# Performance work log

Hardware: AMD Instinct MI355X
Metric: run time of the kernel (lower is better)

The kernel has to match this reference:

```python
import jax, jax.numpy as jnp
import numpy as np

DIM = 768
NUM_HEADS = 12


def setup_inputs() -> dict:
    key = jax.random.key(0)
    k1, k2, k3 = jax.random.split(key, 3)
    x = jax.random.normal(k1, (8, 32, 32, DIM), dtype=jnp.float32)
    # xavier_uniform-style init for kernels
    lim_qkv = float(np.sqrt(6.0 / (DIM + 3 * DIM)))
    lim_o = float(np.sqrt(6.0 / (DIM + DIM)))
    w_qkv = jax.random.uniform(k2, (DIM, 3 * DIM), jnp.float32, -lim_qkv, lim_qkv)
    w_o = jax.random.uniform(k3, (DIM, DIM), jnp.float32, -lim_o, lim_o)
    return {"x": x, "w_qkv": w_qkv, "w_o": w_o}


def reference(x, w_qkv, w_o):
    bs, h, w, c = x.shape
    n = h * w
    nh = NUM_HEADS
    hd = c // nh
    xt = x.reshape(bs, n, c)
    qkv = xt @ w_qkv                                   # [bs, n, 3c]
    qkv = qkv.reshape(bs, n, 3, nh, hd)
    qkv = jnp.transpose(qkv, (2, 0, 3, 1, 4))          # [3, bs, nh, n, hd]
    q, k, v = qkv[0], qkv[1], qkv[2]
    scale = hd ** -0.5
    attn = jnp.einsum('bhqd,bhkd->bhqk', q, k) * scale  # [bs, nh, n, n]
    attn = jax.nn.softmax(attn, axis=-1)
    out = jnp.einsum('bhqk,bhkd->bhqd', attn, v)       # [bs, nh, n, hd]
    out = out.swapaxes(1, 2).reshape(bs, n, c)
    out = out @ w_o
    side = int(n ** 0.5)
    return out.reshape(bs, side, side, -1)
```

## Files before the change

kernel.cpp:

```cpp
#include <hip/hip_runtime.h>
#include <hip/hip_bf16.h>
#include <stdint.h>
#include <math.h>

#define SEQ   1024
#define NHEAD 12
#define HD    64
#define CDIM  768
#define MTOK  8192
#define NQKV  2304
#define NPAIR 96

#define QSCALE 0.18033688011112042f

typedef uint16_t u16;
typedef __attribute__((ext_vector_type(8)))  __bf16 bf16x8;
typedef __attribute__((ext_vector_type(4)))  float  f32x4;
typedef __attribute__((ext_vector_type(16))) float  f32x16;

__device__ __forceinline__ u16 f32_to_bf16(float f) {
  union { float f; uint32_t u; } cv; cv.f = f;
  uint32_t u = cv.u;
  return (u16)((u + 0x7FFFu + ((u >> 16) & 1u)) >> 16);
}

__device__ __forceinline__ uint32_t cvt_pk_bf16(float lo, float hi) {
  uint32_t r;
  asm("v_cvt_pk_bf16_f32 %0, %1, %2" : "=v"(r) : "v"(lo), "v"(hi));
  return r;
}

__device__ __forceinline__ void pl32_swap(uint32_t& a, uint32_t& b) {
  asm("v_permlane32_swap_b32 %0, %1" : "+v"(a), "+v"(b));
}

__device__ __forceinline__ float vexp2(float x) {
  float r; asm("v_exp_f32 %0, %1" : "=v"(r) : "v"(x)); return r;
}
__device__ __forceinline__ float vmax3(float a, float b, float c) {
  float d; asm("v_max3_f32 %0, %1, %2, %3" : "=v"(d) : "v"(a), "v"(b), "v"(c)); return d;
}
__device__ __forceinline__ float vrcp(float x) {
  float r; asm("v_rcp_f32 %0, %1" : "=v"(r) : "v"(x)); return r;
}

__device__ __forceinline__ void load_lds16(const u16* g, u16* l) {
  __builtin_amdgcn_global_load_lds(
      (const __attribute__((address_space(1))) uint32_t*)g,
      (__attribute__((address_space(3))) uint32_t*)l, 16, 0, 0);
}

__device__ __forceinline__ bf16x8 ldsw(const u16* base, int r, int cb) {
  int byte = (r << 7) + cb;
  byte ^= ((r & 7) << 4);
  return *(const bf16x8*)((const char*)base + byte);
}

template<int NB>
__device__ __forceinline__ void stage_swz(const u16* __restrict__ g, u16* l, int tid) {
  #pragma unroll
  for (int i = 0; i < NB / 4096; ++i) {
    int F = i * 4096 + tid * 16;
    int S = F ^ (((F >> 7) & 7) << 4);
    load_lds16(g + (S >> 1), l + (F >> 1));
  }
}

__device__ __forceinline__ void stage_vt(const u16* __restrict__ vtb, u16* l, int kc, int tid) {
  #pragma unroll
  for (int i = 0; i < 2; ++i) {
    int F = i * 4096 + tid * 16;
    int S = F ^ (((F >> 7) & 7) << 4);
    int r = S >> 7;
    int cb = S & 127;
    load_lds16(vtb + ((size_t)r << 10) + (kc << 6) + (cb >> 1), l + (F >> 1));
  }
}

__global__ __launch_bounds__(256) void cvt_x_kernel(const float* __restrict__ in,
                                                    u16* __restrict__ out) {
  int i = blockIdx.x * 256 + threadIdx.x;
  const float4* p = (const float4*)in + (size_t)i * 2;
  float4 a = p[0], b = p[1];
  uint4 o;
  o.x = cvt_pk_bf16(a.x, a.y);
  o.y = cvt_pk_bf16(a.z, a.w);
  o.z = cvt_pk_bf16(b.x, b.y);
  o.w = cvt_pk_bf16(b.z, b.w);
  ((uint4*)out)[i] = o;
}

__global__ __launch_bounds__(256) void transpose_cvt_kernel(const float* __restrict__ in,
                                                            u16* __restrict__ out,
                                                            int K, int N) {
  __shared__ u16 t[64][66];
  int nbk = K >> 6;
  int bk = blockIdx.x % nbk, bn = blockIdx.x / nbk;
  int k0 = bk << 6, n0 = bn << 6;
  int tid = threadIdx.x;
  #pragma unroll
  for (int i = 0; i < 16; ++i) {
    int idx = i * 256 + tid;
    int kr = idx >> 6, nc = idx & 63;
    t[kr][nc] = f32_to_bf16(in[(size_t)(k0 + kr) * N + n0 + nc]);
  }
  __syncthreads();
  #pragma unroll
  for (int i = 0; i < 16; ++i) {
    int idx = i * 256 + tid;
    int nr = idx >> 6, kc = idx & 63;
    out[(size_t)(n0 + nr) * K + k0 + kc] = t[kc][nr];
  }
}

template<int EPI>
__global__ __launch_bounds__(256) void gemm_bt(const u16* __restrict__ A,
                                               const u16* __restrict__ Bt,
                                               float* __restrict__ Cf,
                                               u16* __restrict__ qb,
                                               u16* __restrict__ kb,
                                               u16* __restrict__ vb,
                                               int M, int N, int K) {
  __shared__ u16 SH[4][8192];

  int bid = blockIdx.x;
  int xcd = bid & 7, ii = bid >> 3;
  int tn = ii >> 3;
  int tm = (xcd << 3) + (ii & 7);
  int mBase = tm << 7, nBase = tn << 7;
  int tid = threadIdx.x;
  int lane = tid & 63, wid = tid >> 6;
  int wr = (wid >> 1) << 6, wc = (wid & 1) << 6;
  int lr = lane & 15, lk = lane >> 4;

  const int nk = K >> 6;

  auto STAGE = [&](int kt, int b) {
    #pragma unroll
    for (int i2 = 0; i2 < 4; ++i2) {
      int F = i2 * 4096 + tid * 16;
      int row = F >> 7;
      int cb  = (F & 127) ^ ((row & 7) << 4);
      load_lds16(A + (size_t)(mBase + row) * K + kt * 64 + (cb >> 1), &SH[b][F >> 1]);
    }
    #pragma unroll
    for (int i2 = 0; i2 < 4; ++i2) {
      int F = i2 * 4096 + tid * 16;
      int row = F >> 7;
      int cb  = (F & 127) ^ ((row & 7) << 4);
      load_lds16(Bt + (size_t)(nBase + row) * K + kt * 64 + (cb >> 1), &SH[2 + b][F >> 1]);
    }
  };

  f32x4 acc[4][4] = {};

  STAGE(0, 0);
  for (int kt = 0; kt < nk; ++kt) {
    const int cur = kt & 1;
    if (kt + 1 < nk) {
      STAGE(kt + 1, cur ^ 1);
      asm volatile("s_waitcnt vmcnt(8)" ::: "memory");
    } else {
      asm volatile("s_waitcnt vmcnt(0)" ::: "memory");
    }
    __builtin_amdgcn_s_barrier();
    asm volatile("" ::: "memory");

    #pragma unroll
    for (int kk = 0; kk < 2; ++kk) {
      bf16x8 af[4], bfr[4];
      #pragma unroll
      for (int i2 = 0; i2 < 4; ++i2)
        af[i2]  = ldsw(SH[cur], wr + i2 * 16 + lr, kk * 64 + lk * 16);
      #pragma unroll
      for (int i2 = 0; i2 < 4; ++i2)
        bfr[i2] = ldsw(SH[2 + cur], wc + i2 * 16 + lr, kk * 64 + lk * 16);
      #pragma unroll
      for (int mi = 0; mi < 4; ++mi)
        #pragma unroll
        for (int ni = 0; ni < 4; ++ni)
          acc[mi][ni] = __builtin_amdgcn_mfma_f32_16x16x32_bf16(af[mi], bfr[ni], acc[mi][ni], 0, 0, 0);
    }

    __builtin_amdgcn_s_barrier();
    asm volatile("" ::: "memory");
  }

  if (EPI == 0) {
    int c0 = nBase + wc;
    int s  = c0 / CDIM;
    int rem0 = c0 - s * CDIM, hh = rem0 >> 6;
    u16* ereg = &SH[0][0] + wid * 4096;

    #pragma unroll
    for (int mi = 0; mi < 4; ++mi)
      #pragma unroll
      for (int ni = 0; ni < 4; ++ni)
        #pragma unroll
        for (int j = 0; j < 4; ++j) {
          float val = acc[mi][ni][j];
          if (s == 0) val *= QSCALE;
          int mloc = mi * 16 + lk * 4 + j;
          int cloc = ni * 16 + lr;
          int rrow = (s == 2) ? cloc : mloc;
          int ccol = (s == 2) ? mloc : cloc;
          int byte = (rrow << 7) + (((ccol << 1)) ^ ((rrow & 7) << 4));
          *(u16*)((char*)ereg + byte) = f32_to_bf16(val);
        }

    u16* dst;
    if (s == 2) {
      int m0 = mBase + wr;
      int bb = m0 >> 10, nn0 = m0 & 1023;
      dst = vb + (((size_t)(bb * NHEAD + hh)) << 16) + ((size_t)lane << 10) + nn0;
    } else {
      int mrow = mBase + wr + lane;
      int bb = mrow >> 10, nn = mrow & 1023;
      u16* buf = (s == 0) ? qb : kb;
      dst = buf + (((size_t)(bb * NHEAD + hh)) << 16) + nn * 64;
    }
    #pragma unroll
    for (int ic = 0; ic < 8; ++ic) {
      int rc = (ic + (lane >> 3)) & 7;
      int byte = (lane << 7) + ((rc << 4) ^ ((lane & 7) << 4));
      bf16x8 vv = *(const bf16x8*)((const char*)ereg + byte);
      *(bf16x8*)(dst + rc * 8) = vv;
    }
  } else {
    char* ereg = (char*)(&SH[0][0]) + wid * 16384;
    #pragma unroll
    for (int mi = 0; mi < 4; ++mi)
      #pragma unroll
      for (int ni = 0; ni < 4; ++ni)
        #pragma unroll
        for (int j = 0; j < 4; ++j) {
          int rrow = mi * 16 + lk * 4 + j;
          int byte = (rrow << 8) + (((ni * 16 + lr) << 2) ^ ((rrow & 7) << 4));
          *(float*)(ereg + byte) = acc[mi][ni][j];
        }
    int mrow = mBase + wr + lane;
    float* dst = Cf + (size_t)mrow * N + (nBase + wc);
    #pragma unroll
    for (int ic = 0; ic < 16; ++ic) {
      int rc = (ic + ((lane >> 3) << 1)) & 15;
      int byte = (lane << 8) + ((rc << 4) ^ ((lane & 7) << 4));
      f32x4 vv = *(const f32x4*)(ereg + byte);
      *(f32x4*)(dst + rc * 4) = vv;
    }
  }
}

__global__ __launch_bounds__(256) void attn_kernel(const u16* __restrict__ q,
                                                   const u16* __restrict__ k,
                                                   const u16* __restrict__ v,
                                                   u16* __restrict__ out) {
  __shared__ u16 Ks[2][64 * 64];
  __shared__ u16 Vs[2][64 * 64];

  int bid = blockIdx.x;
  int wgid = (bid & 7) * 96 + (bid >> 3);
  int pair = wgid >> 3;
  int qt   = wgid & 7;
  int b = pair / NHEAD, hh = pair - b * NHEAD;
  const u16* Kg  = k + ((size_t)pair << 16);
  const u16* Vtb = v + ((size_t)pair << 16);
  int tid = threadIdx.x, lane = tid & 63, wid = tid >> 6;
  int ql = lane & 31, hi = lane >> 5;

  const u16* Qrow = q + ((size_t)pair << 16) + (size_t)((qt << 7) + (wid << 5) + ql) * 64;
  bf16x8 qf[4];
  #pragma unroll
  for (int t = 0; t < 4; ++t)
    qf[t] = *(const bf16x8*)(Qrow + t * 16 + hi * 8);

  bf16x8 onesv;
  { union { uint32_t u[4]; bf16x8 v8; } ou;
    ou.u[0] = ou.u[1] = ou.u[2] = ou.u[3] = 0x3F803F80u; onesv = ou.v8; }

  stage_swz<8192>(Kg, Ks[0], tid);
  stage_vt(Vtb, Vs[0], 0, tid);

  float m_ = -1e30f;
  f32x16 acc0 = {}, acc1 = {};
  f32x16 accL = {};

  for (int kc = 0; kc < 16; ++kc) {
    const int cur = kc & 1;
    if (kc < 15) {
      stage_swz<8192>(Kg + ((kc + 1) << 12), Ks[cur ^ 1], tid);
      stage_vt(Vtb, Vs[cur ^ 1], kc + 1, tid);
      asm volatile("s_waitcnt vmcnt(4)" ::: "memory");
    } else {
      asm volatile("s_waitcnt vmcnt(0)" ::: "memory");
    }
    __builtin_amdgcn_s_barrier();
    asm volatile("" ::: "memory");

    f32x16 s0 = {}, s1 = {};
    __builtin_amdgcn_s_setprio(1);
    #pragma unroll
    for (int t = 0; t < 4; ++t) {
      bf16x8 k0 = ldsw(Ks[cur], ql,      t * 32 + hi * 16);
      s0 = __builtin_amdgcn_mfma_f32_32x32x16_bf16(k0, qf[t], s0, 0, 0, 0);
      bf16x8 k1 = ldsw(Ks[cur], 32 + ql, t * 32 + hi * 16);
      s1 = __builtin_amdgcn_mfma_f32_32x32x16_bf16(k1, qf[t], s1, 0, 0, 0);
    }
    __builtin_amdgcn_s_setprio(0);

    float a0 = vmax3(s0[0],  s0[1],  s0[2]);
    float a1 = vmax3(s0[3],  s0[4],  s0[5]);
    float a2 = vmax3(s0[6],  s0[7],  s0[8]);
    float a3 = vmax3(s0[9],  s0[10], s0[11]);
    float a4 = vmax3(s0[12], s0[13], s0[14]);
    float a5 = vmax3(s0[15], s1[0],  s1[1]);
    float a6 = vmax3(s1[2],  s1[3],  s1[4]);
    float a7 = vmax3(s1[5],  s1[6],  s1[7]);
    float a8 = vmax3(s1[8],  s1[9],  s1[10]);
    float a9 = vmax3(s1[11], s1[12], s1[13]);
    float aA = fmaxf(s1[14], s1[15]);
    float b0 = vmax3(a0, a1, a2);
    float b1 = vmax3(a3, a4, a5);
    float b2 = vmax3(a6, a7, a8);
    float b3 = vmax3(a9, aA, b0);
    float pm = vmax3(b1, b2, b3);

    if (!__all(pm - m_ <= 8.f)) {
      float om = fmaxf(pm, __shfl_xor(pm, 32, 64));
      float newm = fmaxf(m_, om);
      float alpha = vexp2(m_ - newm);
      m_ = newm;
      #pragma unroll
      for (int r = 0; r < 16; ++r) {
        int qr = (r & 3) + 8 * (r >> 2) + 4 * hi;
        float ar = __shfl(alpha, qr, 32);
        acc0[r] *= ar;
        acc1[r] *= ar;
        accL[r] *= ar;
      }
    }

    f32x16 mv;
    #pragma unroll
    for (int r = 0; r < 16; ++r) mv[r] = m_;
    f32x16 d0 = s0 - mv, d1 = s1 - mv;
    #pragma unroll
    for (int r = 0; r < 16; ++r) s0[r] = vexp2(d0[r]);
    #pragma unroll
    for (int r = 0; r < 16; ++r) s1[r] = vexp2(d1[r]);

    __builtin_amdgcn_s_setprio(1);
    #pragma unroll
    for (int t = 0; t < 4; ++t) {
      const int base = (t & 1) * 8;
      uint32_t wA, wB, wC, wD;
      if (t < 2) {
        wA = cvt_pk_bf16(s0[base + 0], s0[base + 1]);
        wB = cvt_pk_bf16(s0[base + 2], s0[base + 3]);
        wC = cvt_pk_bf16(s0[base + 4], s0[base + 5]);
        wD = cvt_pk_bf16(s0[base + 6], s0[base + 7]);
      } else {
        wA = cvt_pk_bf16(s1[base + 0], s1[base + 1]);
        wB = cvt_pk_bf16(s1[base + 2], s1[base + 3]);
        wC = cvt_pk_bf16(s1[base + 4], s1[base + 5]);
        wD = cvt_pk_bf16(s1[base + 6], s1[base + 7]);
      }
      pl32_swap(wA, wC);
      pl32_swap(wB, wD);
      union { uint32_t u[4]; bf16x8 v8; } pu;
      pu.u[0] = wA; pu.u[1] = wB; pu.u[2] = wC; pu.u[3] = wD;
      bf16x8 v0 = ldsw(Vs[cur], ql,      t * 32 + hi * 16);
      acc0 = __builtin_amdgcn_mfma_f32_32x32x16_bf16(pu.v8, v0, acc0, 0, 0, 0);
      bf16x8 v1 = ldsw(Vs[cur], 32 + ql, t * 32 + hi * 16);
      acc1 = __builtin_amdgcn_mfma_f32_32x32x16_bf16(pu.v8, v1, acc1, 0, 0, 0);
      accL = __builtin_amdgcn_mfma_f32_32x32x16_bf16(pu.v8, onesv, accL, 0, 0, 0);
    }
    __builtin_amdgcn_s_setprio(0);

    __builtin_amdgcn_s_barrier();
    asm volatile("" ::: "memory");
  }

  u16* ob = out + ((size_t)(b * SEQ + (qt << 7) + (wid << 5))) * CDIM + hh * 64 + ql;
  #pragma unroll
  for (int r = 0; r < 16; ++r) {
    int qr = (r & 3) + 8 * (r >> 2) + 4 * hi;
    float ilr = vrcp(accL[r]);
    ob[(size_t)qr * CDIM]      = f32_to_bf16(acc0[r] * ilr);
    ob[(size_t)qr * CDIM + 32] = f32_to_bf16(acc1[r] * ilr);
  }
}

extern "C" void kernel_launch(void* const* d_in, const int* in_sizes, int n_in,
                              void* d_out, int out_size, void* d_ws, size_t ws_size,
                              hipStream_t stream) {
  const float* x     = (const float*)d_in[0];
  const float* w_qkv = (const float*)d_in[1];
  const float* w_o   = (const float*)d_in[2];
  float* out = (float*)d_out;

  u16* xb    = (u16*)d_ws;
  u16* wqkvT = xb    + (size_t)MTOK * CDIM;
  u16* woT   = wqkvT + (size_t)NQKV * CDIM;
  u16* qb    = woT   + (size_t)CDIM * CDIM;
  u16* kb    = qb    + (size_t)NPAIR * SEQ * HD;
  u16* vb    = kb    + (size_t)NPAIR * SEQ * HD;
  u16* ao    = vb    + (size_t)NPAIR * SEQ * HD;

  cvt_x_kernel<<<dim3((MTOK * CDIM) / (256 * 8)), 256, 0, stream>>>(x, xb);
  transpose_cvt_kernel<<<dim3((CDIM / 64) * (NQKV / 64)), 256, 0, stream>>>(w_qkv, wqkvT, CDIM, NQKV);
  transpose_cvt_kernel<<<dim3((CDIM / 64) * (CDIM / 64)), 256, 0, stream>>>(w_o, woT, CDIM, CDIM);

  gemm_bt<0><<<dim3((MTOK / 128) * (NQKV / 128)), 256, 0, stream>>>(
      xb, wqkvT, nullptr, qb, kb, vb, MTOK, NQKV, CDIM);

  attn_kernel<<<dim3(NPAIR * 8), 256, 0, stream>>>(qb, kb, vb, ao);

  gemm_bt<1><<<dim3((MTOK / 128) * (CDIM / 128)), 256, 0, stream>>>(
      ao, woT, out, nullptr, nullptr, nullptr, MTOK, CDIM, CDIM);
}
```

Baseline: 133.6 us.

## Software-pipeline attention: overlap next QK^T with previous softmax/PV

Restructures the attention loop so the QK^T MFMAs for one key chunk run in the same barrier interval as the softmax and PV of the previous chunk, using two sets of score registers. V staging moves to a triple buffer so the previous chunk's V tile stays resident while the next one loads. Launch bounds now request 3 blocks per CU. The aim is to hide softmax VALU latency behind matrix work, at the cost of more registers and slightly more LDS, which could reduce occupancy or cause spills.

```diff
diff --git a/kernel.cpp b/kernel.cpp
--- a/kernel.cpp
+++ b/kernel.cpp
@@ -250,12 +250,12 @@
   }
 }
 
-__global__ __launch_bounds__(256) void attn_kernel(const u16* __restrict__ q,
-                                                   const u16* __restrict__ k,
-                                                   const u16* __restrict__ v,
-                                                   u16* __restrict__ out) {
-  __shared__ u16 Ks[2][64 * 64];
-  __shared__ u16 Vs[2][64 * 64];
+__global__ __launch_bounds__(256, 3) void attn_kernel(const u16* __restrict__ q,
+                                                      const u16* __restrict__ k,
+                                                      const u16* __restrict__ v,
+                                                      u16* __restrict__ out) {
+  __shared__ u16 Ks[2][4096];
+  __shared__ u16 Vs[3][4096];
 
   int bid = blockIdx.x;
   int wgid = (bid & 7) * 96 + (bid >> 3);
@@ -277,36 +277,12 @@
   { union { uint32_t u[4]; bf16x8 v8; } ou;
     ou.u[0] = ou.u[1] = ou.u[2] = ou.u[3] = 0x3F803F80u; onesv = ou.v8; }
 
-  stage_swz<8192>(Kg, Ks[0], tid);
-  stage_vt(Vtb, Vs[0], 0, tid);
-
   float m_ = -1e30f;
   f32x16 acc0 = {}, acc1 = {};
   f32x16 accL = {};
-
-  for (int kc = 0; kc < 16; ++kc) {
-    const int cur = kc & 1;
-    if (kc < 15) {
-      stage_swz<8192>(Kg + ((kc + 1) << 12), Ks[cur ^ 1], tid);
-      stage_vt(Vtb, Vs[cur ^ 1], kc + 1, tid);
-      asm volatile("s_waitcnt vmcnt(4)" ::: "memory");
-    } else {
-      asm volatile("s_waitcnt vmcnt(0)" ::: "memory");
-    }
-    __builtin_amdgcn_s_barrier();
-    asm volatile("" ::: "memory");
-
-    f32x16 s0 = {}, s1 = {};
-    __builtin_amdgcn_s_setprio(1);
-    #pragma unroll
-    for (int t = 0; t < 4; ++t) {
-      bf16x8 k0 = ldsw(Ks[cur], ql,      t * 32 + hi * 16);
-      s0 = __builtin_amdgcn_mfma_f32_32x32x16_bf16(k0, qf[t], s0, 0, 0, 0);
-      bf16x8 k1 = ldsw(Ks[cur], 32 + ql, t * 32 + hi * 16);
-      s1 = __builtin_amdgcn_mfma_f32_32x32x16_bf16(k1, qf[t], s1, 0, 0, 0);
-    }
-    __builtin_amdgcn_s_setprio(0);
-
+  f32x16 pA0, pA1, pB0, pB1;
+
+  auto SMPV = [&](f32x16& s0, f32x16& s1, const u16* vbase) {
     float a0 = vmax3(s0[0],  s0[1],  s0[2]);
     float a1 = vmax3(s0[3],  s0[4],  s0[5]);
     float a2 = vmax3(s0[6],  s0[7],  s0[8]);
@@ -368,17 +344,60 @@
       pl32_swap(wB, wD);
       union { uint32_t u[4]; bf16x8 v8; } pu;
       pu.u[0] = wA; pu.u[1] = wB; pu.u[2] = wC; pu.u[3] = wD;
-      bf16x8 v0 = ldsw(Vs[cur], ql,      t * 32 + hi * 16);
+      bf16x8 v0 = ldsw(vbase, ql,      t * 32 + hi * 16);
       acc0 = __builtin_amdgcn_mfma_f32_32x32x16_bf16(pu.v8, v0, acc0, 0, 0, 0);
-      bf16x8 v1 = ldsw(Vs[cur], 32 + ql, t * 32 + hi * 16);
+      bf16x8 v1 = ldsw(vbase, 32 + ql, t * 32 + hi * 16);
       acc1 = __builtin_amdgcn_mfma_f32_32x32x16_bf16(pu.v8, v1, acc1, 0, 0, 0);
       accL = __builtin_amdgcn_mfma_f32_32x32x16_bf16(pu.v8, onesv, accL, 0, 0, 0);
     }
     __builtin_amdgcn_s_setprio(0);
-
+  };
+
+  auto QK = [&](int kc, f32x16& s0, f32x16& s1) {
+    const u16* kbase = Ks[kc & 1];
+    s0 = (f32x16){}; s1 = (f32x16){};
+    __builtin_amdgcn_s_setprio(1);
+    #pragma unroll
+    for (int t = 0; t < 4; ++t) {
+      bf16x8 k0 = ldsw(kbase, ql,      t * 32 + hi * 16);
+      s0 = __builtin_amdgcn_mfma_f32_32x32x16_bf16(k0, qf[t], s0, 0, 0, 0);
+      bf16x8 k1 = ldsw(kbase, 32 + ql, t * 32 + hi * 16);
+      s1 = __builtin_amdgcn_mfma_f32_32x32x16_bf16(k1, qf[t], s1, 0, 0, 0);
+    }
+    __builtin_amdgcn_s_setprio(0);
+  };
+
+  auto TOP = [&](int kc) {
+    if (kc < 15) {
+      int nx = kc + 1;
+      stage_swz<8192>(Kg + (nx << 12), Ks[nx & 1], tid);
+      stage_vt(Vtb, Vs[nx % 3], nx, tid);
+      asm volatile("s_waitcnt vmcnt(4)" ::: "memory");
+    } else {
+      asm volatile("s_waitcnt vmcnt(0)" ::: "memory");
+    }
     __builtin_amdgcn_s_barrier();
     asm volatile("" ::: "memory");
-  }
+  };
+  auto BOT = [&]() {
+    __builtin_amdgcn_s_barrier();
+    asm volatile("" ::: "memory");
+  };
+
+  stage_swz<8192>(Kg, Ks[0], tid);
+  stage_vt(Vtb, Vs[0], 0, tid);
+
+  for (int kc2 = 0; kc2 < 16; kc2 += 2) {
+    TOP(kc2);
+    QK(kc2, pA0, pA1);
+    if (kc2 > 0) SMPV(pB0, pB1, Vs[(kc2 + 2) % 3]);
+    BOT();
+    TOP(kc2 + 1);
+    QK(kc2 + 1, pB0, pB1);
+    SMPV(pA0, pA1, Vs[kc2 % 3]);
+    BOT();
+  }
+  SMPV(pB0, pB1, Vs[0]);
 
   u16* ob = out + ((size_t)(b * SEQ + (qt << 7) + (wid << 5))) * CDIM + hh * 64 + ql;
   #pragma unroll
```

New measurement: 125.4 us. -6.1%, faster.
